# Performance work log

Measured on AMD Instinct MI355X. Metric: run time of the kernel, lower is better.

Reference implementation:

```python
import jax, jax.numpy as jnp
import numpy as np

N_NODES, N_EDGES, HIDDEN, N_LAYERS, VOCAB = 50000, 800000, 64, 2, 100

def silu(v):
    return v * jax.nn.sigmoid(v)

def setup_inputs() -> dict:
    key = jax.random.key(0)
    ks = jax.random.split(key, 18)
    N, E, H, L = N_NODES, N_EDGES, HIDDEN, N_LAYERS
    atomic_numbers = jax.random.randint(ks[0], (N,), 0, VOCAB)
    pos = jax.random.normal(ks[1], (N, 3), jnp.float32)
    edge_index = jax.random.randint(ks[2], (2, E), 0, N)
    edge_attr = jax.random.normal(ks[3], (E, 4), jnp.float32)
    emb = (jax.random.normal(ks[4], (VOCAB, H), jnp.float32) * 0.1).at[0].set(0.0)  # padding_idx=0
    def w(k, shape):
        return jax.random.normal(k, shape, jnp.float32) * (1.0 / np.sqrt(shape[-2]))
    return {
        'atomic_numbers': atomic_numbers, 'pos': pos,
        'edge_index': edge_index, 'edge_attr': edge_attr, 'emb': emb,
        # phi_e: Linear(2H+1,H) -> SiLU -> Linear(H,H) -> SiLU, stacked over layers
        'e_w1': w(ks[5], (L, 2 * H + 1, H)), 'e_b1': jnp.zeros((L, H), jnp.float32),
        'e_w2': w(ks[6], (L, H, H)),         'e_b2': jnp.zeros((L, H), jnp.float32),
        # phi_h: Linear(2H,H) -> SiLU -> Linear(H,H)
        'h_w1': w(ks[7], (L, 2 * H, H)),     'h_b1': jnp.zeros((L, H), jnp.float32),
        'h_w2': w(ks[8], (L, H, H)),         'h_b2': jnp.zeros((L, H), jnp.float32),
        # phi_x: Linear(H,H) -> SiLU -> Linear(H,1)
        'x_w1': w(ks[9], (L, H, H)),         'x_b1': jnp.zeros((L, H), jnp.float32),
        'x_w2': w(ks[10], (L, H, 1)),        'x_b2': jnp.zeros((L, 1), jnp.float32),
    }

def reference(atomic_numbers, pos, edge_index, edge_attr, emb,
              e_w1, e_b1, e_w2, e_b2, h_w1, h_b1, h_w2, h_b2,
              x_w1, x_b1, x_w2, x_b2):
    N = pos.shape[0]
    src, dst = edge_index[0], edge_index[1]  # PyG: h_j = h[src], h_i = h[dst]; aggregate to dst
    h = emb[atomic_numbers]  # [N, H]
    x = pos
    for l in range(N_LAYERS):
        x_diff = x[src] - x[dst]                       # [E, 3]
        r_ij = jnp.linalg.norm(x_diff, axis=-1, keepdims=True)  # [E, 1]
        feat = jnp.concatenate([h[dst], h[src], r_ij], axis=-1)  # [E, 2H+1]
        m_ij = silu(silu(feat @ e_w1[l] + e_b1[l]) @ e_w2[l] + e_b2[l])  # [E, H]
        W_ij = silu(m_ij @ x_w1[l] + x_b1[l]) @ x_w2[l] + x_b2[l]        # [E, 1]
        x = x + jax.ops.segment_sum(W_ij * x_diff, dst, num_segments=N)
        m_i = jax.ops.segment_sum(m_ij, dst, num_segments=N)             # [N, H]
        hm = jnp.concatenate([h, m_i], axis=-1)                          # [N, 2H]
        h = h + (silu(hm @ h_w1[l] + h_b1[l]) @ h_w2[l] + h_b2[l])
    return h, x
```

## Files before the change

kernel.cpp:

```cpp
#include <hip/hip_runtime.h>

#define NN 50000
#define NE 800000
#define HD 64
#define NL 2
#define NT_E (NE / 16)
#define NT_N (NN / 16)
#define NCH 196

typedef __attribute__((ext_vector_type(4))) float f32x4;
typedef __attribute__((ext_vector_type(8))) short s16x8;

#define FLAG_OFF 0
#define WB_OFF   16
#define EMB_O 0
#define EW1_O 6400
#define EB1_O 22912
#define EW2_O 23040
#define EB2_O 31232
#define HW1_O 31360
#define HB1_O 47744
#define HW2_O 47872
#define HB2_O 56064
#define XW1_O 56192
#define XB1_O 64384
#define XW2_O 64512
#define XB2_O 64640
#define X_OFF    (WB_OFF + 64656)
#define MAGG_OFF (X_OFF + NN * 4)
#define XAGG_OFF (MAGG_OFF + NN * HD)
#define HBF_OFF  (XAGG_OFF + NN * 3)
#define CNT_OFF  (HBF_OFF + NN * 32)
#define CSUM_OFF (CNT_OFF + NCH * 256)
#define INCL_OFF (CSUM_OFF + 256)
#define PAIR_OFF (INCL_OFF + NCH * 256)

#define ROWP 72

__device__ __forceinline__ float bf2f(unsigned short u) {
    return __uint_as_float(((unsigned int)u) << 16);
}
__device__ __forceinline__ unsigned short f2bf(float f) {
    unsigned int i = __float_as_uint(f);
    i += 0x7fffu + ((i >> 16) & 1u);
    return (unsigned short)(i >> 16);
}
__device__ __forceinline__ unsigned short f2bf_t(float f) {
    return (unsigned short)(__float_as_uint(f) >> 16);
}
__device__ __forceinline__ float silu(float v) {
    const float e = __expf(-v);
    return v * __builtin_amdgcn_rcpf(1.0f + e);
}
__device__ __forceinline__ float ldf(const void* p, int i, int bf) {
    return bf ? bf2f(((const unsigned short*)p)[i]) : ((const float*)p)[i];
}

__global__ void detect_kernel(const unsigned short* __restrict__ pos, int* __restrict__ flag) {
    const int lane = threadIdx.x;
    const float v = bf2f(pos[2 * lane]);
    const float a = fabsf(v);
    const int ok = (a >= 1e-6f && a <= 1e6f) ? 1 : 0;
    const unsigned long long m = __ballot(ok);
    if (lane == 0) *flag = (__popcll(m) >= 32) ? 1 : 0;
}

__global__ __launch_bounds__(256) void convert_kernel(
    const void* pos, const void* emb,
    const void* ew1, const void* eb1, const void* ew2, const void* eb2,
    const void* hw1, const void* hb1, const void* hw2, const void* hb2,
    const void* xw1, const void* xb1, const void* xw2, const void* xb2,
    float* __restrict__ wbuf, float* __restrict__ x, const int* __restrict__ flag)
{
    const int bf = *flag;
    const int tid = blockIdx.x * blockDim.x + threadIdx.x;
    const int stride = gridDim.x * blockDim.x;
    for (int n = tid; n < NN; n += stride) {
        x[n * 4 + 0] = ldf(pos, n * 3 + 0, bf);
        x[n * 4 + 1] = ldf(pos, n * 3 + 1, bf);
        x[n * 4 + 2] = ldf(pos, n * 3 + 2, bf);
        x[n * 4 + 3] = 0.f;
    }
    for (int i = tid; i < 6400; i += stride) wbuf[EMB_O + i] = ldf(emb, i, bf);
    for (int i = tid; i < 16512; i += stride) wbuf[EW1_O + i] = ldf(ew1, i, bf);
    for (int i = tid; i < 128; i += stride) wbuf[EB1_O + i] = ldf(eb1, i, bf);
    for (int i = tid; i < 8192; i += stride) wbuf[EW2_O + i] = ldf(ew2, i, bf);
    for (int i = tid; i < 128; i += stride) wbuf[EB2_O + i] = ldf(eb2, i, bf);
    for (int i = tid; i < 16384; i += stride) wbuf[HW1_O + i] = ldf(hw1, i, bf);
    for (int i = tid; i < 128; i += stride) wbuf[HB1_O + i] = ldf(hb1, i, bf);
    for (int i = tid; i < 8192; i += stride) wbuf[HW2_O + i] = ldf(hw2, i, bf);
    for (int i = tid; i < 128; i += stride) wbuf[HB2_O + i] = ldf(hb2, i, bf);
    for (int i = tid; i < 8192; i += stride) wbuf[XW1_O + i] = ldf(xw1, i, bf);
    for (int i = tid; i < 128; i += stride) wbuf[XB1_O + i] = ldf(xb1, i, bf);
    for (int i = tid; i < 128; i += stride) wbuf[XW2_O + i] = ldf(xw2, i, bf);
    for (int i = tid; i < 2; i += stride) wbuf[XB2_O + i] = ldf(xb2, i, bf);
}

__global__ __launch_bounds__(256) void init_h_kernel(
    const int* __restrict__ an, const float* __restrict__ embf,
    unsigned short* __restrict__ h_bf)
{
    const int stride = gridDim.x * blockDim.x;
    for (int i = blockIdx.x * blockDim.x + threadIdx.x; i < NN * HD; i += stride) {
        int a = an[i >> 6];
        a = (a < 0) ? 0 : (a > 99 ? 99 : a);
        h_bf[i] = f2bf(embf[a * HD + (i & 63)]);
    }
}

__global__ __launch_bounds__(256) void hist_kernel(const int* __restrict__ ei, int* __restrict__ cnt) {
    const int stride = gridDim.x * blockDim.x;
    for (int e = blockIdx.x * blockDim.x + threadIdx.x; e < NE; e += stride) {
        int d = ei[NE + e];
        d = (d < 0) ? 0 : (d >= NN ? NN - 1 : d);
        atomicAdd(&cnt[d], 1);
    }
}

__global__ __launch_bounds__(256) void scan1_kernel(
    const int* __restrict__ cnt, int* __restrict__ incl, int* __restrict__ csum)
{
    __shared__ int s[256];
    const int t = threadIdx.x, b = blockIdx.x, i = b * 256 + t;
    s[t] = cnt[i];
    __syncthreads();
#pragma unroll
    for (int o = 1; o < 256; o <<= 1) {
        const int u = (t >= o) ? s[t - o] : 0;
        __syncthreads();
        s[t] += u;
        __syncthreads();
    }
    incl[i] = s[t];
    if (t == 255) csum[b] = s[255];
}

__global__ void scan2_kernel(int* __restrict__ csum) {
    __shared__ int s[256];
    const int t = threadIdx.x;
    s[t] = (t < NCH) ? csum[t] : 0;
    __syncthreads();
#pragma unroll
    for (int o = 1; o < 256; o <<= 1) {
        const int u = (t >= o) ? s[t - o] : 0;
        __syncthreads();
        s[t] += u;
        __syncthreads();
    }
    if (t < NCH) csum[t] = s[t];
}

__global__ __launch_bounds__(256) void scan3_kernel(
    int* __restrict__ cnt, const int* __restrict__ incl, const int* __restrict__ csum)
{
    const int t = threadIdx.x, b = blockIdx.x, i = b * 256 + t;
    const int off = (b > 0) ? csum[b - 1] : 0;
    cnt[i] = incl[i] - cnt[i] + off;
}

__global__ __launch_bounds__(256) void scatter_kernel(
    const int* __restrict__ ei, int* __restrict__ cur, int2* __restrict__ pair)
{
    const int stride = gridDim.x * blockDim.x;
    for (int e = blockIdx.x * blockDim.x + threadIdx.x; e < NE; e += stride) {
        int s = ei[e];
        int d = ei[NE + e];
        s = (s < 0) ? 0 : (s >= NN ? NN - 1 : s);
        d = (d < 0) ? 0 : (d >= NN ? NN - 1 : d);
        const int p = atomicAdd(&cur[d], 1);
        pair[p] = make_int2(s, d);
    }
}

__global__ __launch_bounds__(256, 4) void edge_mfma_kernel(
    const unsigned short* __restrict__ h_bf, const float* __restrict__ x,
    const int2* __restrict__ pair,
    const float* __restrict__ w1, const float* __restrict__ b1,
    const float* __restrict__ b2,
    const float* __restrict__ w2,
    const float* __restrict__ xw1, const float* __restrict__ xb1,
    const float* __restrict__ xw2, const float* __restrict__ xb2,
    float* __restrict__ m_agg, float* __restrict__ x_agg)
{
    __shared__ unsigned short s_w1p[4 * 4 * 64 * 8];
    __shared__ unsigned short s_xw1p[2 * 4 * 64 * 8];
    __shared__ unsigned short s_act[4][16 * ROWP];
    __shared__ float s_xd[4][16][4];
    __shared__ float s_wv[4][16];

    const int tid = threadIdx.x;
    for (int p = tid; p < 4 * 4 * 64 * 8; p += 256) {
        const int j = p & 7, ln = (p >> 3) & 63, nt = (p >> 9) & 3, kc = p >> 11;
        const int k = kc * 32 + (ln >> 4) * 8 + j, n = nt * 16 + (ln & 15);
        s_w1p[p] = f2bf(w1[k * 64 + n]);
    }
    for (int p = tid; p < 2 * 4 * 64 * 8; p += 256) {
        const int j = p & 7, ln = (p >> 3) & 63, nt = (p >> 9) & 3, kc = p >> 11;
        const int k = kc * 32 + (ln >> 4) * 8 + j, n = nt * 16 + (ln & 15);
        s_xw1p[p] = f2bf(xw1[k * 64 + n]);
    }
    __syncthreads();

    const int lane = tid & 63;
    const int wid = tid >> 6;
    const int l15 = lane & 15;
    const int q = lane >> 4;

    s16x8 bw2[2][4];
#pragma unroll
    for (int kc = 0; kc < 2; ++kc)
#pragma unroll
        for (int nt = 0; nt < 4; ++nt)
#pragma unroll
            for (int j = 0; j < 8; ++j)
                bw2[kc][nt][j] = (short)f2bf(w2[(kc * 32 + q * 8 + j) * 64 + nt * 16 + l15]);

    float b1v[4], b2v[4], xb1v[4], xw2v[4], wrv[4];
#pragma unroll
    for (int nt = 0; nt < 4; ++nt) {
        b1v[nt] = b1[nt * 16 + l15];
        b2v[nt] = b2[nt * 16 + l15];
        xb1v[nt] = xb1[nt * 16 + l15];
        xw2v[nt] = xw2[nt * 16 + l15];
        wrv[nt] = w1[128 * 64 + nt * 16 + l15];
    }
    const float xb2v = xb2[0];

    unsigned short* act = s_act[wid];
    float (*xd)[4] = s_xd[wid];
    float* wv = s_wv[wid];

    const int gwave = (blockIdx.x << 2) + wid;
    const int nwaves = gridDim.x << 2;

    for (int t = gwave; t < NT_E; t += nwaves) {
        const int e0 = t * 16;
        const int2 e = pair[e0 + l15];
        const int sidx = e.x, didx = e.y;
        const f32x4 xs = *(const f32x4*)&x[sidx * 4];
        const f32x4 xdv = *(const f32x4*)&x[didx * 4];
        const float ax = xs[0] - xdv[0];
        const float ay = xs[1] - xdv[1];
        const float az = xs[2] - xdv[2];
        const float rme = sqrtf(ax * ax + ay * ay + az * az);
        if (lane < 16) { xd[lane][0] = ax; xd[lane][1] = ay; xd[lane][2] = az; }

        const s16x8 a_hd0 = *(const s16x8*)&h_bf[didx * 64 + q * 8];
        const s16x8 a_hd1 = *(const s16x8*)&h_bf[didx * 64 + 32 + q * 8];
        const s16x8 a_hs0 = *(const s16x8*)&h_bf[sidx * 64 + q * 8];
        const s16x8 a_hs1 = *(const s16x8*)&h_bf[sidx * 64 + 32 + q * 8];

        f32x4 acc[4];
#pragma unroll
        for (int nt = 0; nt < 4; ++nt) acc[nt] = (f32x4){0.f, 0.f, 0.f, 0.f};
#pragma unroll
        for (int kc = 0; kc < 4; ++kc) {
            const s16x8 a = (kc == 0) ? a_hd0 : (kc == 1) ? a_hd1 : (kc == 2) ? a_hs0 : a_hs1;
#pragma unroll
            for (int nt = 0; nt < 4; ++nt) {
                const s16x8 b = *(const s16x8*)&s_w1p[((kc * 4 + nt) * 64 + lane) * 8];
                acc[nt] = __builtin_amdgcn_mfma_f32_16x16x32_bf16(a, b, acc[nt], 0, 0, 0);
            }
        }
        float rv[4];
#pragma unroll
        for (int r = 0; r < 4; ++r) rv[r] = __shfl(rme, q * 4 + r, 64);
#pragma unroll
        for (int nt = 0; nt < 4; ++nt)
#pragma unroll
            for (int r = 0; r < 4; ++r) {
                const float v = silu(acc[nt][r] + b1v[nt] + rv[r] * wrv[nt]);
                act[(q * 4 + r) * ROWP + nt * 16 + l15] = f2bf_t(v);
            }

        f32x4 acc2[4];
#pragma unroll
        for (int nt = 0; nt < 4; ++nt) acc2[nt] = (f32x4){0.f, 0.f, 0.f, 0.f};
#pragma unroll
        for (int kc = 0; kc < 2; ++kc) {
            const s16x8 a = *(const s16x8*)&act[l15 * ROWP + kc * 32 + q * 8];
#pragma unroll
            for (int nt = 0; nt < 4; ++nt)
                acc2[nt] = __builtin_amdgcn_mfma_f32_16x16x32_bf16(a, bw2[kc][nt], acc2[nt], 0, 0, 0);
        }
#pragma unroll
        for (int nt = 0; nt < 4; ++nt)
#pragma unroll
            for (int r = 0; r < 4; ++r) {
                const float v = silu(acc2[nt][r] + b2v[nt]);
                act[(q * 4 + r) * ROWP + nt * 16 + l15] = f2bf_t(v);
            }

        f32x4 xacc[4];
#pragma unroll
        for (int nt = 0; nt < 4; ++nt) xacc[nt] = (f32x4){0.f, 0.f, 0.f, 0.f};
#pragma unroll
        for (int kc = 0; kc < 2; ++kc) {
            const s16x8 a = *(const s16x8*)&act[l15 * ROWP + kc * 32 + q * 8];
#pragma unroll
            for (int nt = 0; nt < 4; ++nt) {
                const s16x8 b = *(const s16x8*)&s_xw1p[((kc * 4 + nt) * 64 + lane) * 8];
                xacc[nt] = __builtin_amdgcn_mfma_f32_16x16x32_bf16(a, b, xacc[nt], 0, 0, 0);
            }
        }
        float ssum[4];
#pragma unroll
        for (int r = 0; r < 4; ++r) {
            float s = 0.f;
#pragma unroll
            for (int nt = 0; nt < 4; ++nt)
                s += silu(xacc[nt][r] + xb1v[nt]) * xw2v[nt];
            ssum[r] = s;
        }
#pragma unroll
        for (int off = 1; off < 16; off <<= 1)
#pragma unroll
            for (int r = 0; r < 4; ++r) ssum[r] += __shfl_xor(ssum[r], off, 64);
        if (l15 == 0) {
#pragma unroll
            for (int r = 0; r < 4; ++r) wv[q * 4 + r] = ssum[r] + xb2v;
        }

        int dstv[17];
#pragma unroll
        for (int rr = 0; rr < 16; ++rr) dstv[rr] = __shfl(didx, rr, 64);
        dstv[16] = -1;

        float macc = 0.f;
#pragma unroll
        for (int rr = 0; rr < 16; ++rr) {
            macc += bf2f(act[rr * ROWP + lane]);
            if (dstv[rr + 1] != dstv[rr]) {
                atomicAdd(&m_agg[dstv[rr] * 64 + lane], macc);
                macc = 0.f;
            }
        }
        if (lane < 3) {
            float xac = 0.f;
#pragma unroll
            for (int rr = 0; rr < 16; ++rr) {
                xac += wv[rr] * xd[rr][lane];
                if (dstv[rr + 1] != dstv[rr]) {
                    atomicAdd(&x_agg[dstv[rr] * 3 + lane], xac);
                    xac = 0.f;
                }
            }
        }
    }
}

__global__ __launch_bounds__(256, 4) void node_mfma_kernel(
    float* __restrict__ x,
    const float* __restrict__ m_agg, const float* __restrict__ x_agg,
    const float* __restrict__ w1, const float* __restrict__ b1,
    const float* __restrict__ w2, const float* __restrict__ b2,
    unsigned short* __restrict__ h_bf,
    void* __restrict__ outv, const int* __restrict__ flag)
{
    __shared__ unsigned short s_w1p[4 * 4 * 64 * 8];
    __shared__ unsigned short s_act[4][16 * ROWP];

    const int tid = threadIdx.x;
    for (int p = tid; p < 4 * 4 * 64 * 8; p += 256) {
        const int j = p & 7, ln = (p >> 3) & 63, nt = (p >> 9) & 3, kc = p >> 11;
        const int k = kc * 32 + (ln >> 4) * 8 + j, n = nt * 16 + (ln & 15);
        s_w1p[p] = f2bf(w1[k * 64 + n]);
    }
    __syncthreads();

    const int bf = flag ? *flag : 1;
    const int lane = tid & 63;
    const int wid = tid >> 6;
    const int l15 = lane & 15;
    const int q = lane >> 4;

    for (int n = blockIdx.x * 256 + tid; n < NN; n += gridDim.x * 256) {
#pragma unroll
        for (int c = 0; c < 3; ++c) {
            const float xn = x[n * 4 + c] + x_agg[n * 3 + c];
            x[n * 4 + c] = xn;
            if (outv) {
                if (bf) ((unsigned short*)outv)[NN * HD + n * 3 + c] = f2bf(xn);
                else ((float*)outv)[NN * HD + n * 3 + c] = xn;
            }
        }
    }

    s16x8 bw2[2][4];
#pragma unroll
    for (int kc = 0; kc < 2; ++kc)
#pragma unroll
        for (int nt = 0; nt < 4; ++nt)
#pragma unroll
            for (int j = 0; j < 8; ++j)
                bw2[kc][nt][j] = (short)f2bf(w2[(kc * 32 + q * 8 + j) * 64 + nt * 16 + l15]);

    float b1v[4], b2v[4];
#pragma unroll
    for (int nt = 0; nt < 4; ++nt) {
        b1v[nt] = b1[nt * 16 + l15];
        b2v[nt] = b2[nt * 16 + l15];
    }
    unsigned short* act = s_act[wid];

    for (int t = (blockIdx.x << 2) + wid; t < NT_N; t += gridDim.x << 2) {
        const int n = t * 16 + l15;
        const s16x8 a0 = *(const s16x8*)&h_bf[n * 64 + q * 8];
        const s16x8 a1 = *(const s16x8*)&h_bf[n * 64 + 32 + q * 8];
        const f32x4 m0 = *(const f32x4*)&m_agg[n * 64 + q * 8];
        const f32x4 m1 = *(const f32x4*)&m_agg[n * 64 + q * 8 + 4];
        const f32x4 m2 = *(const f32x4*)&m_agg[n * 64 + 32 + q * 8];
        const f32x4 m3 = *(const f32x4*)&m_agg[n * 64 + 32 + q * 8 + 4];
        s16x8 a2, a3;
#pragma unroll
        for (int j = 0; j < 4; ++j) {
            a2[j] = (short)f2bf(m0[j]); a2[4 + j] = (short)f2bf(m1[j]);
            a3[j] = (short)f2bf(m2[j]); a3[4 + j] = (short)f2bf(m3[j]);
        }

        f32x4 acc[4];
#pragma unroll
        for (int nt = 0; nt < 4; ++nt) acc[nt] = (f32x4){0.f, 0.f, 0.f, 0.f};
#pragma unroll
        for (int kc = 0; kc < 4; ++kc) {
            const s16x8 a = (kc == 0) ? a0 : (kc == 1) ? a1 : (kc == 2) ? a2 : a3;
#pragma unroll
            for (int nt = 0; nt < 4; ++nt) {
                const s16x8 b = *(const s16x8*)&s_w1p[((kc * 4 + nt) * 64 + lane) * 8];
                acc[nt] = __builtin_amdgcn_mfma_f32_16x16x32_bf16(a, b, acc[nt], 0, 0, 0);
            }
        }
#pragma unroll
        for (int nt = 0; nt < 4; ++nt)
#pragma unroll
            for (int r = 0; r < 4; ++r)
                act[(q * 4 + r) * ROWP + nt * 16 + l15] = f2bf_t(silu(acc[nt][r] + b1v[nt]));

        f32x4 acc2[4];
#pragma unroll
        for (int nt = 0; nt < 4; ++nt) acc2[nt] = (f32x4){0.f, 0.f, 0.f, 0.f};
#pragma unroll
        for (int kc = 0; kc < 2; ++kc) {
            const s16x8 a = *(const s16x8*)&act[l15 * ROWP + kc * 32 + q * 8];
#pragma unroll
            for (int nt = 0; nt < 4; ++nt)
                acc2[nt] = __builtin_amdgcn_mfma_f32_16x16x32_bf16(a, bw2[kc][nt], acc2[nt], 0, 0, 0);
        }
#pragma unroll
        for (int nt = 0; nt < 4; ++nt)
#pragma unroll
            for (int r = 0; r < 4; ++r) {
                const int row = t * 16 + q * 4 + r, col = nt * 16 + l15;
                const float hn = bf2f(h_bf[row * 64 + col]) + acc2[nt][r] + b2v[nt];
                h_bf[row * 64 + col] = f2bf(hn);
                if (outv) {
                    if (bf) ((unsigned short*)outv)[row * 64 + col] = f2bf(hn);
                    else ((float*)outv)[row * 64 + col] = hn;
                }
            }
    }
}

extern "C" void kernel_launch(void* const* d_in, const int* in_sizes, int n_in,
                              void* d_out, int out_size, void* d_ws, size_t ws_size,
                              hipStream_t stream) {
    const int* an = (const int*)d_in[0];
    const void* pos = d_in[1];
    const int* ei = (const int*)d_in[2];

    int wi = 4;
    if (n_in > 4 && in_sizes[4] == 6400) wi = 4;
    else if (n_in > 3 && in_sizes[3] == 6400) wi = 3;
    const void* emb = d_in[wi];
    const void* e_w1 = d_in[wi + 1];
    const void* e_b1 = d_in[wi + 2];
    const void* e_w2 = d_in[wi + 3];
    const void* e_b2 = d_in[wi + 4];
    const void* h_w1 = d_in[wi + 5];
    const void* h_b1 = d_in[wi + 6];
    const void* h_w2 = d_in[wi + 7];
    const void* h_b2 = d_in[wi + 8];
    const void* x_w1 = d_in[wi + 9];
    const void* x_b1 = d_in[wi + 10];
    const void* x_w2 = d_in[wi + 11];
    const void* x_b2 = d_in[wi + 12];

    float* ws = (float*)d_ws;
    int* flag = (int*)(ws + FLAG_OFF);
    float* wbuf = ws + WB_OFF;
    float* x = ws + X_OFF;
    float* m_agg = ws + MAGG_OFF;
    float* x_agg = ws + XAGG_OFF;
    unsigned short* h_bf = (unsigned short*)(ws + HBF_OFF);
    int* cnt = (int*)(ws + CNT_OFF);
    int* csum = (int*)(ws + CSUM_OFF);
    int* incl = (int*)(ws + INCL_OFF);
    int2* pair = (int2*)(ws + PAIR_OFF);

    detect_kernel<<<1, 64, 0, stream>>>((const unsigned short*)pos, flag);
    convert_kernel<<<256, 256, 0, stream>>>(pos, emb,
        e_w1, e_b1, e_w2, e_b2, h_w1, h_b1, h_w2, h_b2,
        x_w1, x_b1, x_w2, x_b2, wbuf, x, flag);
    init_h_kernel<<<784, 256, 0, stream>>>(an, wbuf + EMB_O, h_bf);

    hipMemsetAsync(cnt, 0, NCH * 256 * sizeof(int), stream);
    hist_kernel<<<512, 256, 0, stream>>>(ei, cnt);
    scan1_kernel<<<NCH, 256, 0, stream>>>(cnt, incl, csum);
    scan2_kernel<<<1, 256, 0, stream>>>(csum);
    scan3_kernel<<<NCH, 256, 0, stream>>>(cnt, incl, csum);
    scatter_kernel<<<512, 256, 0, stream>>>(ei, cnt, pair);

    for (int l = 0; l < NL; ++l) {
        hipMemsetAsync(m_agg, 0, (size_t)NN * HD * sizeof(float), stream);
        hipMemsetAsync(x_agg, 0, (size_t)NN * 3 * sizeof(float), stream);

        edge_mfma_kernel<<<1024, 256, 0, stream>>>(h_bf, x, pair,
            wbuf + EW1_O + l * 129 * 64, wbuf + EB1_O + l * 64,
            wbuf + EB2_O + l * 64,
            wbuf + EW2_O + l * 64 * 64,
            wbuf + XW1_O + l * 64 * 64, wbuf + XB1_O + l * 64,
            wbuf + XW2_O + l * 64, wbuf + XB2_O + l,
            m_agg, x_agg);

        void* out_p = (l == NL - 1) ? d_out : nullptr;
        node_mfma_kernel<<<782, 256, 0, stream>>>(x, m_agg, x_agg,
            wbuf + HW1_O + l * 128 * 64, wbuf + HB1_O + l * 64,
            wbuf + HW2_O + l * 64 * 64, wbuf + HB2_O + l * 64,
            h_bf, out_p, flag);
    }
}
```

Before: 448.2 us.

## Fuse edge and node MLPs into one per-node-tile layer kernel with LDS aggregation

```diff
diff --git a/kernel.cpp b/kernel.cpp
--- a/kernel.cpp
+++ b/kernel.cpp
@@ -4,7 +4,6 @@
 #define NE 800000
 #define HD 64
 #define NL 2
-#define NT_E (NE / 16)
 #define NT_N (NN / 16)
 #define NCH 196
 
@@ -26,16 +25,17 @@
 #define XB1_O 64384
 #define XW2_O 64512
 #define XB2_O 64640
-#define X_OFF    (WB_OFF + 64656)
-#define MAGG_OFF (X_OFF + NN * 4)
-#define XAGG_OFF (MAGG_OFF + NN * HD)
-#define HBF_OFF  (XAGG_OFF + NN * 3)
-#define CNT_OFF  (HBF_OFF + NN * 32)
+#define X0_OFF   (WB_OFF + 64656)
+#define X1_OFF   (X0_OFF + NN * 4)
+#define HBF0_OFF (X1_OFF + NN * 4)
+#define HBF1_OFF (HBF0_OFF + NN * 32)
+#define CNT_OFF  (HBF1_OFF + NN * 32)
 #define CSUM_OFF (CNT_OFF + NCH * 256)
 #define INCL_OFF (CSUM_OFF + 256)
 #define PAIR_OFF (INCL_OFF + NCH * 256)
 
 #define ROWP 72
+#define MPITCH 68
 
 __device__ __forceinline__ float bf2f(unsigned short u) {
     return __uint_as_float(((unsigned int)u) << 16);
@@ -70,16 +70,16 @@
     const void* ew1, const void* eb1, const void* ew2, const void* eb2,
     const void* hw1, const void* hb1, const void* hw2, const void* hb2,
     const void* xw1, const void* xb1, const void* xw2, const void* xb2,
-    float* __restrict__ wbuf, float* __restrict__ x, const int* __restrict__ flag)
+    float* __restrict__ wbuf, float* __restrict__ x0, const int* __restrict__ flag)
 {
     const int bf = *flag;
     const int tid = blockIdx.x * blockDim.x + threadIdx.x;
     const int stride = gridDim.x * blockDim.x;
     for (int n = tid; n < NN; n += stride) {
-        x[n * 4 + 0] = ldf(pos, n * 3 + 0, bf);
-        x[n * 4 + 1] = ldf(pos, n * 3 + 1, bf);
-        x[n * 4 + 2] = ldf(pos, n * 3 + 2, bf);
-        x[n * 4 + 3] = 0.f;
+        x0[n * 4 + 0] = ldf(pos, n * 3 + 0, bf);
+        x0[n * 4 + 1] = ldf(pos, n * 3 + 1, bf);
+        x0[n * 4 + 2] = ldf(pos, n * 3 + 2, bf);
+        x0[n * 4 + 3] = 0.f;
     }
     for (int i = tid; i < 6400; i += stride) wbuf[EMB_O + i] = ldf(emb, i, bf);
     for (int i = tid; i < 16512; i += stride) wbuf[EW1_O + i] = ldf(ew1, i, bf);
@@ -151,11 +151,13 @@
 }
 
 __global__ __launch_bounds__(256) void scan3_kernel(
-    int* __restrict__ cnt, const int* __restrict__ incl, const int* __restrict__ csum)
+    int* __restrict__ cnt, int* __restrict__ incl, const int* __restrict__ csum)
 {
     const int t = threadIdx.x, b = blockIdx.x, i = b * 256 + t;
     const int off = (b > 0) ? csum[b - 1] : 0;
-    cnt[i] = incl[i] - cnt[i] + off;
+    const int inc = incl[i] + off;
+    incl[i] = inc;
+    cnt[i] = inc - cnt[i];
 }
 
 __global__ __launch_bounds__(256) void scatter_kernel(
@@ -172,83 +174,98 @@
     }
 }
 
-__global__ __launch_bounds__(256, 4) void edge_mfma_kernel(
-    const unsigned short* __restrict__ h_bf, const float* __restrict__ x,
-    const int2* __restrict__ pair,
-    const float* __restrict__ w1, const float* __restrict__ b1,
-    const float* __restrict__ b2,
-    const float* __restrict__ w2,
+__global__ __launch_bounds__(256, 3) void fused_layer_kernel(
+    const unsigned short* __restrict__ h_in, unsigned short* __restrict__ h_out,
+    const float* __restrict__ x_in, float* __restrict__ x_out,
+    const int2* __restrict__ pair, const int* __restrict__ incl,
+    const float* __restrict__ ew1, const float* __restrict__ eb1,
+    const float* __restrict__ ew2, const float* __restrict__ eb2,
     const float* __restrict__ xw1, const float* __restrict__ xb1,
     const float* __restrict__ xw2, const float* __restrict__ xb2,
-    float* __restrict__ m_agg, float* __restrict__ x_agg)
-{
-    __shared__ unsigned short s_w1p[4 * 4 * 64 * 8];
-    __shared__ unsigned short s_xw1p[2 * 4 * 64 * 8];
+    const float* __restrict__ hw1, const float* __restrict__ hb1,
+    const float* __restrict__ hw2, const float* __restrict__ hb2,
+    void* __restrict__ outv, const int* __restrict__ flag)
+{
+    __shared__ unsigned short s_ew1p[4 * 4 * 64 * 8];
+    __shared__ unsigned short s_hw1p[4 * 4 * 64 * 8];
     __shared__ unsigned short s_act[4][16 * ROWP];
+    __shared__ float s_macc[16 * MPITCH];
+    __shared__ float s_xacc[16 * 4];
     __shared__ float s_xd[4][16][4];
-    __shared__ float s_wv[4][16];
 
     const int tid = threadIdx.x;
-    for (int p = tid; p < 4 * 4 * 64 * 8; p += 256) {
-        const int j = p & 7, ln = (p >> 3) & 63, nt = (p >> 9) & 3, kc = p >> 11;
-        const int k = kc * 32 + (ln >> 4) * 8 + j, n = nt * 16 + (ln & 15);
-        s_w1p[p] = f2bf(w1[k * 64 + n]);
-    }
-    for (int p = tid; p < 2 * 4 * 64 * 8; p += 256) {
-        const int j = p & 7, ln = (p >> 3) & 63, nt = (p >> 9) & 3, kc = p >> 11;
-        const int k = kc * 32 + (ln >> 4) * 8 + j, n = nt * 16 + (ln & 15);
-        s_xw1p[p] = f2bf(xw1[k * 64 + n]);
-    }
-    __syncthreads();
-
     const int lane = tid & 63;
     const int wid = tid >> 6;
     const int l15 = lane & 15;
     const int q = lane >> 4;
-
-    s16x8 bw2[2][4];
+    const int t = blockIdx.x;
+    const int n0 = t * 16;
+
+    for (int p = tid; p < 4 * 4 * 64 * 8; p += 256) {
+        const int j = p & 7, ln = (p >> 3) & 63, nt = (p >> 9) & 3, kc = p >> 11;
+        const int k = kc * 32 + (ln >> 4) * 8 + j, n = nt * 16 + (ln & 15);
+        s_ew1p[p] = f2bf(ew1[k * 64 + n]);
+        s_hw1p[p] = f2bf(hw1[k * 64 + n]);
+    }
+    for (int i = tid; i < 16 * MPITCH; i += 256) s_macc[i] = 0.f;
+    if (tid < 64) s_xacc[tid] = 0.f;
+
+    s16x8 bw2[2][4], bxw1[2][4];
 #pragma unroll
     for (int kc = 0; kc < 2; ++kc)
 #pragma unroll
         for (int nt = 0; nt < 4; ++nt)
 #pragma unroll
-            for (int j = 0; j < 8; ++j)
-                bw2[kc][nt][j] = (short)f2bf(w2[(kc * 32 + q * 8 + j) * 64 + nt * 16 + l15]);
+            for (int j = 0; j < 8; ++j) {
+                const int wi = (kc * 32 + q * 8 + j) * 64 + nt * 16 + l15;
+                bw2[kc][nt][j] = (short)f2bf(ew2[wi]);
+                bxw1[kc][nt][j] = (short)f2bf(xw1[wi]);
+            }
+    const int ncol = wid * 16 + l15;
+    s16x8 bhw2[2];
+#pragma unroll
+    for (int kc = 0; kc < 2; ++kc)
+#pragma unroll
+        for (int j = 0; j < 8; ++j)
+            bhw2[kc][j] = (short)f2bf(hw2[(kc * 32 + q * 8 + j) * 64 + ncol]);
 
     float b1v[4], b2v[4], xb1v[4], xw2v[4], wrv[4];
 #pragma unroll
     for (int nt = 0; nt < 4; ++nt) {
-        b1v[nt] = b1[nt * 16 + l15];
-        b2v[nt] = b2[nt * 16 + l15];
+        b1v[nt] = eb1[nt * 16 + l15];
+        b2v[nt] = eb2[nt * 16 + l15];
         xb1v[nt] = xb1[nt * 16 + l15];
         xw2v[nt] = xw2[nt * 16 + l15];
-        wrv[nt] = w1[128 * 64 + nt * 16 + l15];
+        wrv[nt] = ew1[128 * 64 + nt * 16 + l15];
     }
     const float xb2v = xb2[0];
+    const float hb1v = hb1[ncol], hb2v = hb2[ncol];
+
+    __syncthreads();
 
     unsigned short* act = s_act[wid];
     float (*xd)[4] = s_xd[wid];
-    float* wv = s_wv[wid];
-
-    const int gwave = (blockIdx.x << 2) + wid;
-    const int nwaves = gridDim.x << 2;
-
-    for (int t = gwave; t < NT_E; t += nwaves) {
-        const int e0 = t * 16;
-        const int2 e = pair[e0 + l15];
-        const int sidx = e.x, didx = e.y;
-        const f32x4 xs = *(const f32x4*)&x[sidx * 4];
-        const f32x4 xdv = *(const f32x4*)&x[didx * 4];
+
+    const int e_start = (t == 0) ? 0 : incl[n0 - 1];
+    const int e_end = incl[n0 + 15];
+
+    for (int ce = e_start + wid * 16; ce < e_end; ce += 64) {
+        const int nv = e_end - ce;
+        const int idx = ce + l15;
+        const int2 epr = pair[(idx < e_end) ? idx : (e_end - 1)];
+        const int sidx = epr.x, didx = epr.y;
+        const f32x4 xs = *(const f32x4*)&x_in[sidx * 4];
+        const f32x4 xdv = *(const f32x4*)&x_in[didx * 4];
         const float ax = xs[0] - xdv[0];
         const float ay = xs[1] - xdv[1];
         const float az = xs[2] - xdv[2];
         const float rme = sqrtf(ax * ax + ay * ay + az * az);
         if (lane < 16) { xd[lane][0] = ax; xd[lane][1] = ay; xd[lane][2] = az; }
 
-        const s16x8 a_hd0 = *(const s16x8*)&h_bf[didx * 64 + q * 8];
-        const s16x8 a_hd1 = *(const s16x8*)&h_bf[didx * 64 + 32 + q * 8];
-        const s16x8 a_hs0 = *(const s16x8*)&h_bf[sidx * 64 + q * 8];
-        const s16x8 a_hs1 = *(const s16x8*)&h_bf[sidx * 64 + 32 + q * 8];
+        const s16x8 a_hd0 = *(const s16x8*)&h_in[didx * 64 + q * 8];
+        const s16x8 a_hd1 = *(const s16x8*)&h_in[didx * 64 + 32 + q * 8];
+        const s16x8 a_hs0 = *(const s16x8*)&h_in[sidx * 64 + q * 8];
+        const s16x8 a_hs1 = *(const s16x8*)&h_in[sidx * 64 + 32 + q * 8];
 
         f32x4 acc[4];
 #pragma unroll
@@ -258,13 +275,18 @@
             const s16x8 a = (kc == 0) ? a_hd0 : (kc == 1) ? a_hd1 : (kc == 2) ? a_hs0 : a_hs1;
 #pragma unroll
             for (int nt = 0; nt < 4; ++nt) {
-                const s16x8 b = *(const s16x8*)&s_w1p[((kc * 4 + nt) * 64 + lane) * 8];
+                const s16x8 b = *(const s16x8*)&s_ew1p[((kc * 4 + nt) * 64 + lane) * 8];
                 acc[nt] = __builtin_amdgcn_mfma_f32_16x16x32_bf16(a, b, acc[nt], 0, 0, 0);
             }
         }
         float rv[4];
-#pragma unroll
-        for (int r = 0; r < 4; ++r) rv[r] = __shfl(rme, q * 4 + r, 64);
+        int dsh[4], vr[4];
+#pragma unroll
+        for (int r = 0; r < 4; ++r) {
+            rv[r] = __shfl(rme, q * 4 + r, 64);
+            dsh[r] = __shfl(didx, q * 4 + r, 64) - n0;
+            vr[r] = (q * 4 + r) < nv;
+        }
 #pragma unroll
         for (int nt = 0; nt < 4; ++nt)
 #pragma unroll
@@ -289,6 +311,7 @@
             for (int r = 0; r < 4; ++r) {
                 const float v = silu(acc2[nt][r] + b2v[nt]);
                 act[(q * 4 + r) * ROWP + nt * 16 + l15] = f2bf_t(v);
+                if (vr[r]) atomicAdd(&s_macc[dsh[r] * MPITCH + nt * 16 + l15], v);
             }
 
         f32x4 xacc[4];
@@ -298,10 +321,8 @@
         for (int kc = 0; kc < 2; ++kc) {
             const s16x8 a = *(const s16x8*)&act[l15 * ROWP + kc * 32 + q * 8];
 #pragma unroll
-            for (int nt = 0; nt < 4; ++nt) {
-                const s16x8 b = *(const s16x8*)&s_xw1p[((kc * 4 + nt) * 64 + lane) * 8];
-                xacc[nt] = __builtin_amdgcn_mfma_f32_16x16x32_bf16(a, b, xacc[nt], 0, 0, 0);
-            }
+            for (int nt = 0; nt < 4; ++nt)
+                xacc[nt] = __builtin_amdgcn_mfma_f32_16x16x32_bf16(a, bxw1[kc][nt], xacc[nt], 0, 0, 0);
         }
         float ssum[4];
 #pragma unroll
@@ -316,148 +337,71 @@
         for (int off = 1; off < 16; off <<= 1)
 #pragma unroll
             for (int r = 0; r < 4; ++r) ssum[r] += __shfl_xor(ssum[r], off, 64);
-        if (l15 == 0) {
-#pragma unroll
-            for (int r = 0; r < 4; ++r) wv[q * 4 + r] = ssum[r] + xb2v;
-        }
-
-        int dstv[17];
-#pragma unroll
-        for (int rr = 0; rr < 16; ++rr) dstv[rr] = __shfl(didx, rr, 64);
-        dstv[16] = -1;
-
-        float macc = 0.f;
-#pragma unroll
-        for (int rr = 0; rr < 16; ++rr) {
-            macc += bf2f(act[rr * ROWP + lane]);
-            if (dstv[rr + 1] != dstv[rr]) {
-                atomicAdd(&m_agg[dstv[rr] * 64 + lane], macc);
-                macc = 0.f;
-            }
-        }
-        if (lane < 3) {
-            float xac = 0.f;
-#pragma unroll
-            for (int rr = 0; rr < 16; ++rr) {
-                xac += wv[rr] * xd[rr][lane];
-                if (dstv[rr + 1] != dstv[rr]) {
-                    atomicAdd(&x_agg[dstv[rr] * 3 + lane], xac);
-                    xac = 0.f;
+        if (l15 < 3) {
+#pragma unroll
+            for (int r = 0; r < 4; ++r) {
+                if (vr[r]) {
+                    const float W = ssum[r] + xb2v;
+                    atomicAdd(&s_xacc[dsh[r] * 4 + l15], W * xd[q * 4 + r][l15]);
                 }
             }
         }
     }
-}
-
-__global__ __launch_bounds__(256, 4) void node_mfma_kernel(
-    float* __restrict__ x,
-    const float* __restrict__ m_agg, const float* __restrict__ x_agg,
-    const float* __restrict__ w1, const float* __restrict__ b1,
-    const float* __restrict__ w2, const float* __restrict__ b2,
-    unsigned short* __restrict__ h_bf,
-    void* __restrict__ outv, const int* __restrict__ flag)
-{
-    __shared__ unsigned short s_w1p[4 * 4 * 64 * 8];
-    __shared__ unsigned short s_act[4][16 * ROWP];
-
-    const int tid = threadIdx.x;
-    for (int p = tid; p < 4 * 4 * 64 * 8; p += 256) {
-        const int j = p & 7, ln = (p >> 3) & 63, nt = (p >> 9) & 3, kc = p >> 11;
-        const int k = kc * 32 + (ln >> 4) * 8 + j, n = nt * 16 + (ln & 15);
-        s_w1p[p] = f2bf(w1[k * 64 + n]);
-    }
     __syncthreads();
 
-    const int bf = flag ? *flag : 1;
-    const int lane = tid & 63;
-    const int wid = tid >> 6;
-    const int l15 = lane & 15;
-    const int q = lane >> 4;
-
-    for (int n = blockIdx.x * 256 + tid; n < NN; n += gridDim.x * 256) {
-#pragma unroll
-        for (int c = 0; c < 3; ++c) {
-            const float xn = x[n * 4 + c] + x_agg[n * 3 + c];
-            x[n * 4 + c] = xn;
-            if (outv) {
-                if (bf) ((unsigned short*)outv)[NN * HD + n * 3 + c] = f2bf(xn);
-                else ((float*)outv)[NN * HD + n * 3 + c] = xn;
-            }
-        }
-    }
-
-    s16x8 bw2[2][4];
-#pragma unroll
-    for (int kc = 0; kc < 2; ++kc)
-#pragma unroll
-        for (int nt = 0; nt < 4; ++nt)
-#pragma unroll
-            for (int j = 0; j < 8; ++j)
-                bw2[kc][nt][j] = (short)f2bf(w2[(kc * 32 + q * 8 + j) * 64 + nt * 16 + l15]);
-
-    float b1v[4], b2v[4];
-#pragma unroll
-    for (int nt = 0; nt < 4; ++nt) {
-        b1v[nt] = b1[nt * 16 + l15];
-        b2v[nt] = b2[nt * 16 + l15];
-    }
-    unsigned short* act = s_act[wid];
-
-    for (int t = (blockIdx.x << 2) + wid; t < NT_N; t += gridDim.x << 2) {
-        const int n = t * 16 + l15;
-        const s16x8 a0 = *(const s16x8*)&h_bf[n * 64 + q * 8];
-        const s16x8 a1 = *(const s16x8*)&h_bf[n * 64 + 32 + q * 8];
-        const f32x4 m0 = *(const f32x4*)&m_agg[n * 64 + q * 8];
-        const f32x4 m1 = *(const f32x4*)&m_agg[n * 64 + q * 8 + 4];
-        const f32x4 m2 = *(const f32x4*)&m_agg[n * 64 + 32 + q * 8];
-        const f32x4 m3 = *(const f32x4*)&m_agg[n * 64 + 32 + q * 8 + 4];
-        s16x8 a2, a3;
-#pragma unroll
-        for (int j = 0; j < 4; ++j) {
-            a2[j] = (short)f2bf(m0[j]); a2[4 + j] = (short)f2bf(m1[j]);
-            a3[j] = (short)f2bf(m2[j]); a3[4 + j] = (short)f2bf(m3[j]);
-        }
-
-        f32x4 acc[4];
-#pragma unroll
-        for (int nt = 0; nt < 4; ++nt) acc[nt] = (f32x4){0.f, 0.f, 0.f, 0.f};
-#pragma unroll
-        for (int kc = 0; kc < 4; ++kc) {
-            const s16x8 a = (kc == 0) ? a0 : (kc == 1) ? a1 : (kc == 2) ? a2 : a3;
-#pragma unroll
-            for (int nt = 0; nt < 4; ++nt) {
-                const s16x8 b = *(const s16x8*)&s_w1p[((kc * 4 + nt) * 64 + lane) * 8];
-                acc[nt] = __builtin_amdgcn_mfma_f32_16x16x32_bf16(a, b, acc[nt], 0, 0, 0);
-            }
-        }
-#pragma unroll
-        for (int nt = 0; nt < 4; ++nt)
-#pragma unroll
-            for (int r = 0; r < 4; ++r)
-                act[(q * 4 + r) * ROWP + nt * 16 + l15] = f2bf_t(silu(acc[nt][r] + b1v[nt]));
-
-        f32x4 acc2[4];
-#pragma unroll
-        for (int nt = 0; nt < 4; ++nt) acc2[nt] = (f32x4){0.f, 0.f, 0.f, 0.f};
-#pragma unroll
-        for (int kc = 0; kc < 2; ++kc) {
-            const s16x8 a = *(const s16x8*)&act[l15 * ROWP + kc * 32 + q * 8];
-#pragma unroll
-            for (int nt = 0; nt < 4; ++nt)
-                acc2[nt] = __builtin_amdgcn_mfma_f32_16x16x32_bf16(a, bw2[kc][nt], acc2[nt], 0, 0, 0);
-        }
-#pragma unroll
-        for (int nt = 0; nt < 4; ++nt)
-#pragma unroll
-            for (int r = 0; r < 4; ++r) {
-                const int row = t * 16 + q * 4 + r, col = nt * 16 + l15;
-                const float hn = bf2f(h_bf[row * 64 + col]) + acc2[nt][r] + b2v[nt];
-                h_bf[row * 64 + col] = f2bf(hn);
-                if (outv) {
-                    if (bf) ((unsigned short*)outv)[row * 64 + col] = f2bf(hn);
-                    else ((float*)outv)[row * 64 + col] = hn;
-                }
-            }
+    const int nrow = n0 + l15;
+    const s16x8 ah0 = *(const s16x8*)&h_in[nrow * 64 + q * 8];
+    const s16x8 ah1 = *(const s16x8*)&h_in[nrow * 64 + 32 + q * 8];
+    const f32x4 mm0 = *(const f32x4*)&s_macc[l15 * MPITCH + q * 8];
+    const f32x4 mm1 = *(const f32x4*)&s_macc[l15 * MPITCH + q * 8 + 4];
+    const f32x4 mm2 = *(const f32x4*)&s_macc[l15 * MPITCH + 32 + q * 8];
+    const f32x4 mm3 = *(const f32x4*)&s_macc[l15 * MPITCH + 32 + q * 8 + 4];
+    s16x8 am0, am1;
+#pragma unroll
+    for (int j = 0; j < 4; ++j) {
+        am0[j] = (short)f2bf(mm0[j]); am0[4 + j] = (short)f2bf(mm1[j]);
+        am1[j] = (short)f2bf(mm2[j]); am1[4 + j] = (short)f2bf(mm3[j]);
+    }
+
+    f32x4 nacc = (f32x4){0.f, 0.f, 0.f, 0.f};
+#pragma unroll
+    for (int kc = 0; kc < 4; ++kc) {
+        const s16x8 a = (kc == 0) ? ah0 : (kc == 1) ? ah1 : (kc == 2) ? am0 : am1;
+        const s16x8 b = *(const s16x8*)&s_hw1p[((kc * 4 + wid) * 64 + lane) * 8];
+        nacc = __builtin_amdgcn_mfma_f32_16x16x32_bf16(a, b, nacc, 0, 0, 0);
+    }
+#pragma unroll
+    for (int r = 0; r < 4; ++r)
+        s_act[0][(q * 4 + r) * ROWP + ncol] = f2bf_t(silu(nacc[r] + hb1v));
+    __syncthreads();
+
+    f32x4 nacc2 = (f32x4){0.f, 0.f, 0.f, 0.f};
+#pragma unroll
+    for (int kc = 0; kc < 2; ++kc) {
+        const s16x8 a = *(const s16x8*)&s_act[0][l15 * ROWP + kc * 32 + q * 8];
+        nacc2 = __builtin_amdgcn_mfma_f32_16x16x32_bf16(a, bhw2[kc], nacc2, 0, 0, 0);
+    }
+    const int bfl = flag ? *flag : 1;
+#pragma unroll
+    for (int r = 0; r < 4; ++r) {
+        const int row = n0 + q * 4 + r;
+        const float hn = bf2f(h_in[row * 64 + ncol]) + nacc2[r] + hb2v;
+        h_out[row * 64 + ncol] = f2bf(hn);
+        if (outv) {
+            if (bfl) ((unsigned short*)outv)[row * 64 + ncol] = f2bf(hn);
+            else ((float*)outv)[row * 64 + ncol] = hn;
+        }
+    }
+    if (tid < 48) {
+        const int n = tid / 3, c = tid - n * 3;
+        const float xn = x_in[(n0 + n) * 4 + c] + s_xacc[n * 4 + c];
+        x_out[(n0 + n) * 4 + c] = xn;
+        if (outv) {
+            if (bfl) ((unsigned short*)outv)[NN * HD + (n0 + n) * 3 + c] = f2bf(xn);
+            else ((float*)outv)[NN * HD + (n0 + n) * 3 + c] = xn;
+        }
+    } else if (tid < 64) {
+        x_out[(n0 + (tid - 48)) * 4 + 3] = 0.f;
     }
 }
 
@@ -488,10 +432,10 @@
     float* ws = (float*)d_ws;
     int* flag = (int*)(ws + FLAG_OFF);
     float* wbuf = ws + WB_OFF;
-    float* x = ws + X_OFF;
-    float* m_agg = ws + MAGG_OFF;
-    float* x_agg = ws + XAGG_OFF;
-    unsigned short* h_bf = (unsigned short*)(ws + HBF_OFF);
+    float* x0 = ws + X0_OFF;
+    float* x1 = ws + X1_OFF;
+    unsigned short* h0 = (unsigned short*)(ws + HBF0_OFF);
+    unsigned short* h1 = (unsigned short*)(ws + HBF1_OFF);
     int* cnt = (int*)(ws + CNT_OFF);
     int* csum = (int*)(ws + CSUM_OFF);
     int* incl = (int*)(ws + INCL_OFF);
@@ -500,8 +444,8 @@
     detect_kernel<<<1, 64, 0, stream>>>((const unsigned short*)pos, flag);
     convert_kernel<<<256, 256, 0, stream>>>(pos, emb,
         e_w1, e_b1, e_w2, e_b2, h_w1, h_b1, h_w2, h_b2,
-        x_w1, x_b1, x_w2, x_b2, wbuf, x, flag);
-    init_h_kernel<<<784, 256, 0, stream>>>(an, wbuf + EMB_O, h_bf);
+        x_w1, x_b1, x_w2, x_b2, wbuf, x0, flag);
+    init_h_kernel<<<784, 256, 0, stream>>>(an, wbuf + EMB_O, h0);
 
     hipMemsetAsync(cnt, 0, NCH * 256 * sizeof(int), stream);
     hist_kernel<<<512, 256, 0, stream>>>(ei, cnt);
@@ -511,21 +455,20 @@
     scatter_kernel<<<512, 256, 0, stream>>>(ei, cnt, pair);
 
     for (int l = 0; l < NL; ++l) {
-        hipMemsetAsync(m_agg, 0, (size_t)NN * HD * sizeof(float), stream);
-        hipMemsetAsync(x_agg, 0, (size_t)NN * 3 * sizeof(float), stream);
-
-        edge_mfma_kernel<<<1024, 256, 0, stream>>>(h_bf, x, pair,
+        const unsigned short* hi = (l == 0) ? h0 : h1;
+        unsigned short* ho = (l == 0) ? h1 : h0;
+        const float* xi = (l == 0) ? x0 : x1;
+        float* xo = (l == 0) ? x1 : x0;
+        void* out_p = (l == NL - 1) ? d_out : nullptr;
+
+        fused_layer_kernel<<<NT_N, 256, 0, stream>>>(
+            hi, ho, xi, xo, pair, incl,
             wbuf + EW1_O + l * 129 * 64, wbuf + EB1_O + l * 64,
-            wbuf + EB2_O + l * 64,
-            wbuf + EW2_O + l * 64 * 64,
+            wbuf + EW2_O + l * 64 * 64, wbuf + EB2_O + l * 64,
             wbuf + XW1_O + l * 64 * 64, wbuf + XB1_O + l * 64,
             wbuf + XW2_O + l * 64, wbuf + XB2_O + l,
-            m_agg, x_agg);
-
-        void* out_p = (l == NL - 1) ? d_out : nullptr;
-        node_mfma_kernel<<<782, 256, 0, stream>>>(x, m_agg, x_agg,
             wbuf + HW1_O + l * 128 * 64, wbuf + HB1_O + l * 64,
             wbuf + HW2_O + l * 64 * 64, wbuf + HB2_O + l * 64,
-            h_bf, out_p, flag);
-    }
-}
+            out_p, flag);
+    }
+}
```

Result: slower. 1.128 ms (+151.6%).
